# Performance work log

Measured on AMD Instinct MI355X. Metric: run time of the kernel, lower is better.

## Reference

```python
import jax, jax.numpy as jnp
import numpy as np

E = 100000   # number of edges
S = 64       # multiplicity of 0e (scalar) irreps
V = 32       # multiplicity of 1o (vector) irreps; also number of gates
RS3 = 1.0 / np.sqrt(3.0)   # wigner_3j constant for (1,1,0)/(0,1,1)/(1,0,1) paths
RS6 = 1.0 / np.sqrt(6.0)   # (unused here: no 1o output from 1o x 1o)

# per-path normalization: 1/sqrt(n_paths_to_slot * mul1 * mul2), e3nn-style 'uvw'
A_SS_S = (2.0 * S * S) ** -0.5
A_VV_S = (2.0 * V * V) ** -0.5 * RS3
A_SS_G = (2.0 * S * S) ** -0.5
A_VV_G = (2.0 * V * V) ** -0.5 * RS3
A_SV_V = (2.0 * S * V) ** -0.5 * RS3
A_VS_V = (2.0 * V * S) ** -0.5 * RS3


def setup_inputs() -> dict:
    key = jax.random.key(0)
    ks = jax.random.split(key, 12)
    d_in = S + 3 * V
    return {
        "fea_in1": jax.random.normal(ks[0], (E, d_in), jnp.float32),
        "fea_in2": jax.random.normal(ks[1], (E, d_in), jnp.float32),
        "fea_weight": jax.random.normal(ks[2], (E, V), jnp.float32),   # unused (kept for signature parity)
        "batch_edge": jax.random.randint(ks[3], (E,), 0, 16, jnp.int32),  # unused (norm='')
        # SeparateWeightTensorProduct ('uvw') weights, one tensor per CG path
        "w_ss_s": jax.random.normal(ks[4], (S, S, S), jnp.float32),  # 0e x 0e -> 0e (scalars)
        "w_vv_s": jax.random.normal(ks[5], (V, V, S), jnp.float32),  # 1o x 1o -> 0e (scalars)
        "w_ss_g": jax.random.normal(ks[6], (S, S, V), jnp.float32),  # 0e x 0e -> 0e (gates)
        "w_vv_g": jax.random.normal(ks[7], (V, V, V), jnp.float32),  # 1o x 1o -> 0e (gates)
        "w_sv_v": jax.random.normal(ks[8], (S, V, V), jnp.float32),  # 0e x 1o -> 1o
        "w_vs_v": jax.random.normal(ks[9], (V, S, V), jnp.float32),  # 1o x 0e -> 1o
        # equivariant o3.Linear weights (channel mixing per irrep, shared over m)
        "wl_s": jax.random.normal(ks[10], (S, S), jnp.float32),
        "wl_v": jax.random.normal(ks[11], (V, V), jnp.float32),
    }


def reference(fea_in1, fea_in2, fea_weight, batch_edge,
              w_ss_s, w_vv_s, w_ss_g, w_vv_g, w_sv_v, w_vs_v, wl_s, wl_v):
    # split flattened irreps features: [S scalars | V vectors * 3]
    s1 = fea_in1[:, :S]
    v1 = fea_in1[:, S:].reshape(-1, V, 3)
    s2 = fea_in2[:, :S]
    v2 = fea_in2[:, S:].reshape(-1, V, 3)

    # --- separate-weight tensor product (fully connected 'uvw' paths) ---
    z_s = (A_SS_S * jnp.einsum('uvw,eu,ev->ew', w_ss_s, s1, s2)
           + A_VV_S * jnp.einsum('uvw,eui,evi->ew', w_vv_s, v1, v2))   # (E,S) 0e
    z_g = (A_SS_G * jnp.einsum('uvw,eu,ev->ew', w_ss_g, s1, s2)
           + A_VV_G * jnp.einsum('uvw,eui,evi->ew', w_vv_g, v1, v2))   # (E,V) gates 0e
    z_v = (A_SV_V * jnp.einsum('uvw,eu,evi->ewi', w_sv_v, s1, v2)
           + A_VS_V * jnp.einsum('uvw,eui,ev->ewi', w_vs_v, v1, s2))   # (E,V,3) 1o

    # --- gated nonlinearity: silu on scalars, sigmoid gates on vectors ---
    s_act = jax.nn.silu(z_s)
    v_act = jax.nn.sigmoid(z_g)[:, :, None] * z_v

    # --- equivariant linear (per-irrep channel mixing, fan-in normalized) ---
    s_out = (s_act @ wl_s) * (S ** -0.5)                    # (E,S)
    v_out = jnp.einsum('evi,vw->ewi', v_act, wl_v) * (V ** -0.5)  # (E,V,3)

    return jnp.concatenate([s_out, v_out.reshape(-1, 3 * V)], axis=-1)  # (E, S+3V)
```

## Files before the change

kernel.cpp:

```cpp
#include <hip/hip_runtime.h>


typedef _Float16 f16;
typedef _Float16 f16x8 __attribute__((ext_vector_type(8)));
typedef float    f32x4 __attribute__((ext_vector_type(4)));

constexpr float A_SS  = 0.011048543456039806f;
constexpr float A_VV  = 0.012757759747374832f;
constexpr float A_SV  = 0.009021097956087904f;
constexpr float SO_SC = 0.125f;
constexpr float VO_SC = 0.1767766952966369f;

#define MFMA16(A, B, C) __builtin_amdgcn_mfma_f32_16x16x32_f16((A), (B), (C), 0, 0, 0)

static __device__ __forceinline__ f16x8 splat8(f16 x) {
    return (f16x8){x, x, x, x, x, x, x, x};
}

__global__ void prep_weights(const float* __restrict__ wss_s, const float* __restrict__ wvv_s,
                             const float* __restrict__ wss_g, const float* __restrict__ wvv_g,
                             const float* __restrict__ wsv,   const float* __restrict__ wvs,
                             const float* __restrict__ wls,   const float* __restrict__ wlv,
                             f16* __restrict__ b1p, f16* __restrict__ b2p,
                             f16* __restrict__ wlsP, f16* __restrict__ wlvP)
{
    int idx = blockIdx.x * 256 + threadIdx.x;
    const int N1 = 160 * 6 * 512;
    const int N2 = 128 * 2 * 512;
    const int N3 = 8 * 512;
    const int N4 = 2 * 512;
    if (idx < N1) {
        int j = idx & 7, L = (idx >> 3) & 63, ct = idx >> 9;
        int t = ct % 6, c = ct / 6;
        int k = c * 32 + (L >> 4) * 8 + j;
        int n = t * 16 + (L & 15);
        float val;
        if (k < 4096) { int u = k >> 6, v = k & 63, p = u * 64 + v;
            val = A_SS * (n < 64 ? wss_s[p * 64 + n] : wss_g[p * 32 + (n - 64)]);
        } else { int k2 = k - 4096; int u = k2 >> 5, v = k2 & 31, p = u * 32 + v;
            val = A_VV * (n < 64 ? wvv_s[p * 64 + n] : wvv_g[p * 32 + (n - 64)]);
        }
        b1p[idx] = (f16)val;
    } else if (idx < N1 + N2) {
        int id2 = idx - N1;
        int j = id2 & 7, L = (id2 >> 3) & 63, ct = id2 >> 9;
        int t = ct & 1, c = ct >> 1;
        int k = c * 32 + (L >> 4) * 8 + j;
        int n = t * 16 + (L & 15);
        float val;
        if (k < 2048) { int u = k >> 5, v = k & 31; val = wsv[(u * 32 + v) * 32 + n]; }
        else { int k2 = k - 2048; int u = k2 >> 6, v = k2 & 63; val = wvs[(u * 64 + v) * 32 + n]; }
        b2p[id2] = (f16)(A_SV * val);
    } else if (idx < N1 + N2 + N3) {
        int id3 = idx - N1 - N2;
        int j = id3 & 7, L = (id3 >> 3) & 63, ct = id3 >> 9;
        int t = ct & 3, kc = ct >> 2;
        int k = kc * 32 + (L >> 4) * 8 + j;
        int n = t * 16 + (L & 15);
        wlsP[id3] = (f16)(SO_SC * wls[k * 64 + n]);
    } else if (idx < N1 + N2 + N3 + N4) {
        int id4 = idx - N1 - N2 - N3;
        int j = id4 & 7, L = (id4 >> 3) & 63, t = id4 >> 9;
        int k = (L >> 4) * 8 + j;
        int n = t * 16 + (L & 15);
        wlvP[id4] = (f16)(VO_SC * wlv[k * 32 + n]);
    }
}

__global__ __launch_bounds__(256, 4)
void seconv_mfma(const float* __restrict__ fea1, const float* __restrict__ fea2,
                 const f16* __restrict__ b1p, const f16* __restrict__ b2p,
                 const f16* __restrict__ wlsP, const f16* __restrict__ wlvP,
                 float* __restrict__ out, int E)
{
    __shared__ __align__(128) char smem[40960];
    f16*   zSh  = (f16*)smem;
    f16*   zGh  = (f16*)(smem + 9216);
    f16*   ZVH  = (f16*)(smem + 13568);
    float* OUTV = (float*)smem;

    const int tid  = threadIdx.x;
    const int lane = tid & 63;
    const int m    = lane & 15;
    const int quad = lane >> 4;
    const int w    = tid >> 6;
    const int h    = w & 1;
    const int nh   = w >> 1;
    const int tb   = nh * 3;
    const int e0   = blockIdx.x * 64;

    auto ld8 = [&](int e, int hc) -> f16x8 {
        int b = (e * 640 + hc * 2) ^ ((e & 7) << 4);
        return *(const f16x8*)(smem + b);
    };
    auto st2 = [&](int e, int hc, f16 v) {
        int b = (e * 640 + hc * 2) ^ ((e & 7) << 4);
        *(f16*)(smem + b) = v;
    };

    for (int i = tid; i < 64 * 160; i += 256) {
        int e = i / 160, c = i - e * 160;
        int ge = e0 + e; if (ge >= E) ge = E - 1;
        float a = fea1[ge * 160 + c];
        float b = fea2[ge * 160 + c];
        if (c < 64) { st2(e, c, (f16)a); st2(e, 64 + c, (f16)b); }
        else { int c2 = c - 64; int v = c2 / 3, ii = c2 - v * 3;
               st2(e, 128 + ii * 32 + v, (f16)a);
               st2(e, 224 + ii * 32 + v, (f16)b); }
    }
    __syncthreads();

    const int eA = h * 32 + m;
    const int eB = h * 32 + 16 + m;

    f32x4 acc[2][3];
    #pragma unroll
    for (int p = 0; p < 2; ++p)
        #pragma unroll
        for (int t = 0; t < 3; ++t) acc[p][t] = (f32x4){0.f, 0.f, 0.f, 0.f};

    f32x4 bq[4][3];
    #pragma unroll
    for (int s = 0; s < 4; ++s)
        #pragma unroll
        for (int t = 0; t < 3; ++t)
            bq[s][t] = *(const f32x4*)(b1p + ((s * 6 + tb + t) * 64 + lane) * 8);

    {
        f16x8 s2q[2][2];
        #pragma unroll
        for (int p = 0; p < 2; ++p)
            #pragma unroll
            for (int vh = 0; vh < 2; ++vh)
                s2q[p][vh] = ld8(p ? eB : eA, 64 + vh * 32 + quad * 8);

        for (int ub = 0; ub < 8; ++ub) {
            f16x8 s1Ab = ld8(eA, ub * 8);
            f16x8 s1Bb = ld8(eB, ub * 8);
            #pragma unroll
            for (int uj = 0; uj < 8; ++uj) {
                f16x8 s1A = splat8(s1Ab[uj]);
                f16x8 s1B = splat8(s1Bb[uj]);
                #pragma unroll
                for (int vh = 0; vh < 2; ++vh) {
                    const int clo = uj * 2 + vh;
                    const int slot = clo & 3;
                    f16x8 bb0 = __builtin_bit_cast(f16x8, bq[slot][0]);
                    f16x8 bb1 = __builtin_bit_cast(f16x8, bq[slot][1]);
                    f16x8 bb2 = __builtin_bit_cast(f16x8, bq[slot][2]);
                    int cn = ub * 16 + clo + 4;
                    #pragma unroll
                    for (int t = 0; t < 3; ++t)
                        bq[slot][t] = *(const f32x4*)(b1p + ((cn * 6 + tb + t) * 64 + lane) * 8);
                    f16x8 a0 = s1A * s2q[0][vh];
                    f16x8 a1 = s1B * s2q[1][vh];
                    acc[0][0] = MFMA16(a0, bb0, acc[0][0]);
                    acc[0][1] = MFMA16(a0, bb1, acc[0][1]);
                    acc[0][2] = MFMA16(a0, bb2, acc[0][2]);
                    acc[1][0] = MFMA16(a1, bb0, acc[1][0]);
                    acc[1][1] = MFMA16(a1, bb1, acc[1][1]);
                    acc[1][2] = MFMA16(a1, bb2, acc[1][2]);
                }
            }
        }
    }
    {
        f16x8 v2q[2][3];
        #pragma unroll
        for (int p = 0; p < 2; ++p)
            #pragma unroll
            for (int i3 = 0; i3 < 3; ++i3)
                v2q[p][i3] = ld8(p ? eB : eA, 224 + i3 * 32 + quad * 8);

        for (int ub = 0; ub < 4; ++ub) {
            f16x8 xA[3], xB[3];
            #pragma unroll
            for (int i3 = 0; i3 < 3; ++i3) {
                xA[i3] = ld8(eA, 128 + i3 * 32 + ub * 8);
                xB[i3] = ld8(eB, 128 + i3 * 32 + ub * 8);
            }
            #pragma unroll
            for (int uj = 0; uj < 8; ++uj) {
                const int slot = uj & 3;
                f16x8 a0 = splat8(xA[0][uj]) * v2q[0][0];
                a0 += splat8(xA[1][uj]) * v2q[0][1];
                a0 += splat8(xA[2][uj]) * v2q[0][2];
                f16x8 a1 = splat8(xB[0][uj]) * v2q[1][0];
                a1 += splat8(xB[1][uj]) * v2q[1][1];
                a1 += splat8(xB[2][uj]) * v2q[1][2];
                f16x8 bb0 = __builtin_bit_cast(f16x8, bq[slot][0]);
                f16x8 bb1 = __builtin_bit_cast(f16x8, bq[slot][1]);
                f16x8 bb2 = __builtin_bit_cast(f16x8, bq[slot][2]);
                int cn = 128 + ub * 8 + uj + 4; if (cn > 159) cn = 159;
                #pragma unroll
                for (int t = 0; t < 3; ++t)
                    bq[slot][t] = *(const f32x4*)(b1p + ((cn * 6 + tb + t) * 64 + lane) * 8);
                acc[0][0] = MFMA16(a0, bb0, acc[0][0]);
                acc[0][1] = MFMA16(a0, bb1, acc[0][1]);
                acc[0][2] = MFMA16(a0, bb2, acc[0][2]);
                acc[1][0] = MFMA16(a1, bb0, acc[1][0]);
                acc[1][1] = MFMA16(a1, bb1, acc[1][1]);
                acc[1][2] = MFMA16(a1, bb2, acc[1][2]);
            }
        }
    }

    const int e2 = w * 16 + m;
    f16x8 s2g[2], v2g[3];
    #pragma unroll
    for (int vh = 0; vh < 2; ++vh)
        s2g[vh] = ld8(e2, 64 + vh * 32 + quad * 8);
    #pragma unroll
    for (int i3 = 0; i3 < 3; ++i3)
        v2g[i3] = ld8(e2, 224 + i3 * 32 + quad * 8);

    f32x4 acc2[3][2];
    #pragma unroll
    for (int i3 = 0; i3 < 3; ++i3)
        #pragma unroll
        for (int t = 0; t < 2; ++t) acc2[i3][t] = (f32x4){0.f, 0.f, 0.f, 0.f};

    f32x4 bq2[4][2];
    #pragma unroll
    for (int s = 0; s < 4; ++s)
        #pragma unroll
        for (int t = 0; t < 2; ++t)
            bq2[s][t] = *(const f32x4*)(b2p + ((s * 2 + t) * 64 + lane) * 8);

    for (int ub = 0; ub < 8; ++ub) {
        f16x8 s1b = ld8(e2, ub * 8);
        #pragma unroll
        for (int uj = 0; uj < 8; ++uj) {
            const int slot = uj & 3;
            f16x8 bb0 = __builtin_bit_cast(f16x8, bq2[slot][0]);
            f16x8 bb1 = __builtin_bit_cast(f16x8, bq2[slot][1]);
            int cn = ub * 8 + uj + 4;
            #pragma unroll
            for (int t = 0; t < 2; ++t)
                bq2[slot][t] = *(const f32x4*)(b2p + ((cn * 2 + t) * 64 + lane) * 8);
            f16x8 sxv = splat8(s1b[uj]);
            #pragma unroll
            for (int i3 = 0; i3 < 3; ++i3) {
                f16x8 a = sxv * v2g[i3];
                acc2[i3][0] = MFMA16(a, bb0, acc2[i3][0]);
                acc2[i3][1] = MFMA16(a, bb1, acc2[i3][1]);
            }
        }
    }
    for (int ub = 0; ub < 4; ++ub) {
        f16x8 v1b[3];
        #pragma unroll
        for (int i3 = 0; i3 < 3; ++i3)
            v1b[i3] = ld8(e2, 128 + i3 * 32 + ub * 8);
        #pragma unroll
        for (int uj = 0; uj < 8; ++uj) {
            f16x8 v1s0 = splat8(v1b[0][uj]);
            f16x8 v1s1 = splat8(v1b[1][uj]);
            f16x8 v1s2 = splat8(v1b[2][uj]);
            #pragma unroll
            for (int vh = 0; vh < 2; ++vh) {
                const int slot = (uj * 2 + vh) & 3;
                f16x8 bb0 = __builtin_bit_cast(f16x8, bq2[slot][0]);
                f16x8 bb1 = __builtin_bit_cast(f16x8, bq2[slot][1]);
                int cn = 64 + (ub * 8 + uj) * 2 + vh + 4; if (cn > 127) cn = 127;
                #pragma unroll
                for (int t = 0; t < 2; ++t)
                    bq2[slot][t] = *(const f32x4*)(b2p + ((cn * 2 + t) * 64 + lane) * 8);
                f16x8 a0 = v1s0 * s2g[vh];
                f16x8 a1 = v1s1 * s2g[vh];
                f16x8 a2 = v1s2 * s2g[vh];
                acc2[0][0] = MFMA16(a0, bb0, acc2[0][0]);
                acc2[0][1] = MFMA16(a0, bb1, acc2[0][1]);
                acc2[1][0] = MFMA16(a1, bb0, acc2[1][0]);
                acc2[1][1] = MFMA16(a1, bb1, acc2[1][1]);
                acc2[2][0] = MFMA16(a2, bb0, acc2[2][0]);
                acc2[2][1] = MFMA16(a2, bb1, acc2[2][1]);
            }
        }
    }
    __syncthreads();

    #pragma unroll
    for (int p = 0; p < 2; ++p)
        #pragma unroll
        for (int t = 0; t < 3; ++t) {
            int n = (tb + t) * 16 + m;
            #pragma unroll
            for (int r = 0; r < 4; ++r) {
                int e_loc = h * 32 + p * 16 + quad * 4 + r;
                float z = acc[p][t][r];
                if (n < 64) {
                    float s = z / (1.f + __expf(-z));
                    zSh[e_loc * 72 + n] = (f16)s;
                } else {
                    zGh[e_loc * 34 + (n - 64)] = (f16)z;
                }
            }
        }
    __syncthreads();

    #pragma unroll
    for (int t = 0; t < 2; ++t)
        #pragma unroll
        for (int r = 0; r < 4; ++r) {
            int e_loc = w * 16 + quad * 4 + r;
            float zg = (float)zGh[e_loc * 34 + t * 16 + m];
            float gate = 1.f / (1.f + __expf(-zg));
            #pragma unroll
            for (int i3 = 0; i3 < 3; ++i3)
                ZVH[(i3 * 64 + e_loc) * 40 + t * 16 + m] = (f16)(gate * acc2[i3][t][r]);
        }

    {
        f32x4 accS[4];
        #pragma unroll
        for (int t = 0; t < 4; ++t) accS[t] = (f32x4){0.f, 0.f, 0.f, 0.f};
        #pragma unroll
        for (int kc = 0; kc < 2; ++kc) {
            f16x8 aS = *(const f16x8*)(zSh + (w * 16 + m) * 72 + kc * 32 + quad * 8);
            #pragma unroll
            for (int t = 0; t < 4; ++t) {
                f32x4 braw = *(const f32x4*)(wlsP + ((kc * 4 + t) * 64 + lane) * 8);
                accS[t] = MFMA16(aS, __builtin_bit_cast(f16x8, braw), accS[t]);
            }
        }
        #pragma unroll
        for (int t = 0; t < 4; ++t)
            #pragma unroll
            for (int r = 0; r < 4; ++r) {
                int ge = e0 + w * 16 + quad * 4 + r;
                if (ge < E) out[ge * 160 + t * 16 + m] = accS[t][r];
            }
    }
    {
        f32x4 accV[3][2];
        #pragma unroll
        for (int i3 = 0; i3 < 3; ++i3)
            #pragma unroll
            for (int t = 0; t < 2; ++t) accV[i3][t] = (f32x4){0.f, 0.f, 0.f, 0.f};
        f16x8 bV[2];
        #pragma unroll
        for (int t = 0; t < 2; ++t) {
            f32x4 braw = *(const f32x4*)(wlvP + (t * 64 + lane) * 8);
            bV[t] = __builtin_bit_cast(f16x8, braw);
        }
        #pragma unroll
        for (int i3 = 0; i3 < 3; ++i3) {
            f16x8 aV = *(const f16x8*)(ZVH + (i3 * 64 + w * 16 + m) * 40 + quad * 8);
            #pragma unroll
            for (int t = 0; t < 2; ++t) accV[i3][t] = MFMA16(aV, bV[t], accV[i3][t]);
        }
        __syncthreads();
        #pragma unroll
        for (int i3 = 0; i3 < 3; ++i3)
            #pragma unroll
            for (int t = 0; t < 2; ++t)
                #pragma unroll
                for (int r = 0; r < 4; ++r) {
                    int e_loc = w * 16 + quad * 4 + r;
                    OUTV[e_loc * 100 + (t * 16 + m) * 3 + i3] = accV[i3][t][r];
                }
    }
    __syncthreads();

    for (int i = tid; i < 64 * 96; i += 256) {
        int e = i / 96, c = i - e * 96;
        int ge = e0 + e;
        if (ge < E) out[ge * 160 + 64 + c] = OUTV[e * 100 + c];
    }
}

extern "C" void kernel_launch(void* const* d_in, const int* in_sizes, int n_in,
                              void* d_out, int out_size, void* d_ws, size_t ws_size,
                              hipStream_t stream) {
    const float* fea1  = (const float*)d_in[0];
    const float* fea2  = (const float*)d_in[1];
    const float* wss_s = (const float*)d_in[4];
    const float* wvv_s = (const float*)d_in[5];
    const float* wss_g = (const float*)d_in[6];
    const float* wvv_g = (const float*)d_in[7];
    const float* wsv   = (const float*)d_in[8];
    const float* wvs   = (const float*)d_in[9];
    const float* wls   = (const float*)d_in[10];
    const float* wlv   = (const float*)d_in[11];
    float* out = (float*)d_out;

    f16* b1p  = (f16*)d_ws;
    f16* b2p  = (f16*)((char*)d_ws + 983040);
    f16* wlsP = (f16*)((char*)d_ws + 1245184);
    f16* wlvP = (f16*)((char*)d_ws + 1253376);

    int E = in_sizes[0] / 160;
    int prep_total = 491520 + 131072 + 4096 + 1024;
    prep_weights<<<dim3((prep_total + 255) / 256), dim3(256), 0, stream>>>(
        wss_s, wvv_s, wss_g, wvv_g, wsv, wvs, wls, wlv, b1p, b2p, wlsP, wlvP);
    int grid = (E + 63) / 64;
    seconv_mfma<<<dim3(grid), dim3(256), 0, stream>>>(
        fea1, fea2, b1p, b2p, wlsP, wlvP, out, E);
}
```

Before: 455.3 us.

## Repack B weights per N-half for linear streaming and shallower prefetch

Repacks the first tensor-product weight buffer so each N-half (three 16-wide tiles) is contiguous, and walks both B buffers with an incrementing pointer. This replaces per-chunk index arithmetic and halves the prefetch ring from four slots to two. The vector loop is restructured to load 4-wide f16 chunks. The silu/gate epilogue of the first product is computed into packed registers before the second product starts, which overlaps the transcendental math with other work. Risks include exposed load latency from the shallower prefetch, higher register pressure from the held values, and possible out-of-bounds reads past the end of the buffers on the final prefetch, since the old clamp was removed.

New measurement: 396.7 us. 1.15x faster.

```diff
diff --git a/kernel.cpp b/kernel.cpp
--- a/kernel.cpp
+++ b/kernel.cpp
@@ -2,6 +2,7 @@
 
 
 typedef _Float16 f16;
+typedef _Float16 f16x4 __attribute__((ext_vector_type(4)));
 typedef _Float16 f16x8 __attribute__((ext_vector_type(8)));
 typedef float    f32x4 __attribute__((ext_vector_type(4)));
 
@@ -25,15 +26,16 @@
                              f16* __restrict__ wlsP, f16* __restrict__ wlvP)
 {
     int idx = blockIdx.x * 256 + threadIdx.x;
-    const int N1 = 160 * 6 * 512;
+    const int N1 = 2 * 160 * 3 * 512;
     const int N2 = 128 * 2 * 512;
     const int N3 = 8 * 512;
     const int N4 = 2 * 512;
     if (idx < N1) {
-        int j = idx & 7, L = (idx >> 3) & 63, ct = idx >> 9;
-        int t = ct % 6, c = ct / 6;
+        int j = idx & 7, L = (idx >> 3) & 63, rest = idx >> 9;
+        int t3 = rest % 3, rc = rest / 3;
+        int c = rc % 160, nh2 = rc / 160;
         int k = c * 32 + (L >> 4) * 8 + j;
-        int n = t * 16 + (L & 15);
+        int n = (nh2 * 3 + t3) * 16 + (L & 15);
         float val;
         if (k < 4096) { int u = k >> 6, v = k & 63, p = u * 64 + v;
             val = A_SS * (n < 64 ? wss_s[p * 64 + n] : wss_g[p * 32 + (n - 64)]);
@@ -93,6 +95,10 @@
         int b = (e * 640 + hc * 2) ^ ((e & 7) << 4);
         return *(const f16x8*)(smem + b);
     };
+    auto ld4 = [&](int e, int hc) -> f16x4 {
+        int b = (e * 640 + hc * 2) ^ ((e & 7) << 4);
+        return *(const f16x4*)(smem + b);
+    };
     auto st2 = [&](int e, int hc, f16 v) {
         int b = (e * 640 + hc * 2) ^ ((e & 7) << 4);
         *(f16*)(smem + b) = v;
@@ -119,12 +125,14 @@
         #pragma unroll
         for (int t = 0; t < 3; ++t) acc[p][t] = (f32x4){0.f, 0.f, 0.f, 0.f};
 
-    f32x4 bq[4][3];
-    #pragma unroll
-    for (int s = 0; s < 4; ++s)
-        #pragma unroll
-        for (int t = 0; t < 3; ++t)
-            bq[s][t] = *(const f32x4*)(b1p + ((s * 6 + tb + t) * 64 + lane) * 8);
+    const f16* pB = b1p + __builtin_amdgcn_readfirstlane(nh) * (160 * 3 * 512);
+    f32x4 bq[2][3];
+    #pragma unroll
+    for (int t = 0; t < 3; ++t) bq[0][t] = *(const f32x4*)(pB + t * 512 + lane * 8);
+    pB += 1536;
+    #pragma unroll
+    for (int t = 0; t < 3; ++t) bq[1][t] = *(const f32x4*)(pB + t * 512 + lane * 8);
+    pB += 1536;
 
     {
         f16x8 s2q[2][2];
@@ -143,15 +151,13 @@
                 f16x8 s1B = splat8(s1Bb[uj]);
                 #pragma unroll
                 for (int vh = 0; vh < 2; ++vh) {
-                    const int clo = uj * 2 + vh;
-                    const int slot = clo & 3;
-                    f16x8 bb0 = __builtin_bit_cast(f16x8, bq[slot][0]);
-                    f16x8 bb1 = __builtin_bit_cast(f16x8, bq[slot][1]);
-                    f16x8 bb2 = __builtin_bit_cast(f16x8, bq[slot][2]);
-                    int cn = ub * 16 + clo + 4;
+                    f16x8 bb0 = __builtin_bit_cast(f16x8, bq[vh][0]);
+                    f16x8 bb1 = __builtin_bit_cast(f16x8, bq[vh][1]);
+                    f16x8 bb2 = __builtin_bit_cast(f16x8, bq[vh][2]);
                     #pragma unroll
                     for (int t = 0; t < 3; ++t)
-                        bq[slot][t] = *(const f32x4*)(b1p + ((cn * 6 + tb + t) * 64 + lane) * 8);
+                        bq[vh][t] = *(const f32x4*)(pB + t * 512 + lane * 8);
+                    pB += 1536;
                     f16x8 a0 = s1A * s2q[0][vh];
                     f16x8 a1 = s1B * s2q[1][vh];
                     acc[0][0] = MFMA16(a0, bb0, acc[0][0]);
@@ -172,29 +178,29 @@
             for (int i3 = 0; i3 < 3; ++i3)
                 v2q[p][i3] = ld8(p ? eB : eA, 224 + i3 * 32 + quad * 8);
 
-        for (int ub = 0; ub < 4; ++ub) {
-            f16x8 xA[3], xB[3];
+        for (int ub = 0; ub < 8; ++ub) {
+            f16x4 xA[3], xB[3];
             #pragma unroll
             for (int i3 = 0; i3 < 3; ++i3) {
-                xA[i3] = ld8(eA, 128 + i3 * 32 + ub * 8);
-                xB[i3] = ld8(eB, 128 + i3 * 32 + ub * 8);
-            }
-            #pragma unroll
-            for (int uj = 0; uj < 8; ++uj) {
-                const int slot = uj & 3;
+                xA[i3] = ld4(eA, 128 + i3 * 32 + ub * 4);
+                xB[i3] = ld4(eB, 128 + i3 * 32 + ub * 4);
+            }
+            #pragma unroll
+            for (int uj = 0; uj < 4; ++uj) {
+                const int slot = uj & 1;
+                f16x8 bb0 = __builtin_bit_cast(f16x8, bq[slot][0]);
+                f16x8 bb1 = __builtin_bit_cast(f16x8, bq[slot][1]);
+                f16x8 bb2 = __builtin_bit_cast(f16x8, bq[slot][2]);
+                #pragma unroll
+                for (int t = 0; t < 3; ++t)
+                    bq[slot][t] = *(const f32x4*)(pB + t * 512 + lane * 8);
+                pB += 1536;
                 f16x8 a0 = splat8(xA[0][uj]) * v2q[0][0];
                 a0 += splat8(xA[1][uj]) * v2q[0][1];
                 a0 += splat8(xA[2][uj]) * v2q[0][2];
                 f16x8 a1 = splat8(xB[0][uj]) * v2q[1][0];
                 a1 += splat8(xB[1][uj]) * v2q[1][1];
                 a1 += splat8(xB[2][uj]) * v2q[1][2];
-                f16x8 bb0 = __builtin_bit_cast(f16x8, bq[slot][0]);
-                f16x8 bb1 = __builtin_bit_cast(f16x8, bq[slot][1]);
-                f16x8 bb2 = __builtin_bit_cast(f16x8, bq[slot][2]);
-                int cn = 128 + ub * 8 + uj + 4; if (cn > 159) cn = 159;
-                #pragma unroll
-                for (int t = 0; t < 3; ++t)
-                    bq[slot][t] = *(const f32x4*)(b1p + ((cn * 6 + tb + t) * 64 + lane) * 8);
                 acc[0][0] = MFMA16(a0, bb0, acc[0][0]);
                 acc[0][1] = MFMA16(a0, bb1, acc[0][1]);
                 acc[0][2] = MFMA16(a0, bb2, acc[0][2]);
@@ -205,6 +211,20 @@
         }
     }
 
+    f16x4 zpk[2][3];
+    #pragma unroll
+    for (int p = 0; p < 2; ++p)
+        #pragma unroll
+        for (int t = 0; t < 3; ++t) {
+            int n = (tb + t) * 16 + m;
+            #pragma unroll
+            for (int r = 0; r < 4; ++r) {
+                float z = acc[p][t][r];
+                float vv = (n < 64) ? (z / (1.f + __expf(-z))) : z;
+                zpk[p][t][r] = (f16)vv;
+            }
+        }
+
     const int e2 = w * 16 + m;
     f16x8 s2g[2], v2g[3];
     #pragma unroll
@@ -220,24 +240,26 @@
         #pragma unroll
         for (int t = 0; t < 2; ++t) acc2[i3][t] = (f32x4){0.f, 0.f, 0.f, 0.f};
 
-    f32x4 bq2[4][2];
-    #pragma unroll
-    for (int s = 0; s < 4; ++s)
-        #pragma unroll
-        for (int t = 0; t < 2; ++t)
-            bq2[s][t] = *(const f32x4*)(b2p + ((s * 2 + t) * 64 + lane) * 8);
+    const f16* pB2 = b2p;
+    f32x4 bq2[2][2];
+    #pragma unroll
+    for (int t = 0; t < 2; ++t) bq2[0][t] = *(const f32x4*)(pB2 + t * 512 + lane * 8);
+    pB2 += 1024;
+    #pragma unroll
+    for (int t = 0; t < 2; ++t) bq2[1][t] = *(const f32x4*)(pB2 + t * 512 + lane * 8);
+    pB2 += 1024;
 
     for (int ub = 0; ub < 8; ++ub) {
         f16x8 s1b = ld8(e2, ub * 8);
         #pragma unroll
         for (int uj = 0; uj < 8; ++uj) {
-            const int slot = uj & 3;
+            const int slot = uj & 1;
             f16x8 bb0 = __builtin_bit_cast(f16x8, bq2[slot][0]);
             f16x8 bb1 = __builtin_bit_cast(f16x8, bq2[slot][1]);
-            int cn = ub * 8 + uj + 4;
             #pragma unroll
             for (int t = 0; t < 2; ++t)
-                bq2[slot][t] = *(const f32x4*)(b2p + ((cn * 2 + t) * 64 + lane) * 8);
+                bq2[slot][t] = *(const f32x4*)(pB2 + t * 512 + lane * 8);
+            pB2 += 1024;
             f16x8 sxv = splat8(s1b[uj]);
             #pragma unroll
             for (int i3 = 0; i3 < 3; ++i3) {
@@ -259,13 +281,13 @@
             f16x8 v1s2 = splat8(v1b[2][uj]);
             #pragma unroll
             for (int vh = 0; vh < 2; ++vh) {
-                const int slot = (uj * 2 + vh) & 3;
+                const int slot = vh;
                 f16x8 bb0 = __builtin_bit_cast(f16x8, bq2[slot][0]);
                 f16x8 bb1 = __builtin_bit_cast(f16x8, bq2[slot][1]);
-                int cn = 64 + (ub * 8 + uj) * 2 + vh + 4; if (cn > 127) cn = 127;
                 #pragma unroll
                 for (int t = 0; t < 2; ++t)
-                    bq2[slot][t] = *(const f32x4*)(b2p + ((cn * 2 + t) * 64 + lane) * 8);
+                    bq2[slot][t] = *(const f32x4*)(pB2 + t * 512 + lane * 8);
+                pB2 += 1024;
                 f16x8 a0 = v1s0 * s2g[vh];
                 f16x8 a1 = v1s1 * s2g[vh];
                 f16x8 a2 = v1s2 * s2g[vh];
@@ -288,13 +310,8 @@
             #pragma unroll
             for (int r = 0; r < 4; ++r) {
                 int e_loc = h * 32 + p * 16 + quad * 4 + r;
-                float z = acc[p][t][r];
-                if (n < 64) {
-                    float s = z / (1.f + __expf(-z));
-                    zSh[e_loc * 72 + n] = (f16)s;
-                } else {
-                    zGh[e_loc * 34 + (n - 64)] = (f16)z;
-                }
+                if (n < 64) zSh[e_loc * 72 + n] = zpk[p][t][r];
+                else        zGh[e_loc * 34 + (n - 64)] = zpk[p][t][r];
             }
         }
     __syncthreads();
```
